# Kernel tuning notes

Hardware: AMD Instinct MI355X
Metric: run time of the kernel (lower is better)

The kernel has to match this reference:

```python
import jax, jax.numpy as jnp
import numpy as np

N = 50000
H = 8          # heads
C = 10         # out channels per head
F_IN = 128
NEG_SLOPE = 0.2


def _glorot(key, shape, fan_in):
    return jax.random.normal(key, shape, dtype=jnp.float32) / np.sqrt(fan_in)


def setup_inputs() -> dict:
    key = jax.random.key(0)
    ks = jax.random.split(key, 16)
    x = jax.random.normal(ks[0], (N, F_IN), dtype=jnp.float32)
    edge_index = jax.random.randint(ks[1], (2, 1600000), 0, N, dtype=jnp.int64)
    inp = {"x": x, "edge_index": edge_index}
    dims = [F_IN, H * C, H * C]  # input dim of each of the 3 layers
    k = 2
    for i, din in enumerate(dims):
        inp[f"Wl{i}"] = _glorot(ks[k + 0], (din, H * C), din)
        inp[f"Wr{i}"] = _glorot(ks[k + 1], (din, H * C), din)
        inp[f"att{i}"] = _glorot(ks[k + 2], (H, C), C)
        inp[f"b{i}"] = jnp.zeros((H * C,), dtype=jnp.float32)
        k += 3
    return inp


def gatv2_layer(x, Wl, Wr, att, b, src, dst):
    # GATv2Conv (PyG defaults): separate lin_l/lin_r, e = att . leaky_relu(xl_j + xr_i),
    # segment softmax over incoming edges, scatter-add of alpha * xl_j, concat heads + bias.
    n = x.shape[0]
    xl = (x @ Wl).reshape(n, H, C)
    xr = (x @ Wr).reshape(n, H, C)
    e = jax.nn.leaky_relu(xl[src] + xr[dst], NEG_SLOPE)      # [E, H, C]
    score = jnp.einsum('ehc,hc->eh', e, att)                 # [E, H]
    smax = jax.ops.segment_max(score, dst, num_segments=n)   # [N, H]
    ex = jnp.exp(score - smax[dst])
    denom = jax.ops.segment_sum(ex, dst, num_segments=n)
    alpha = ex / (denom[dst] + 1e-16)                        # [E, H]
    out = jax.ops.segment_sum(alpha[:, :, None] * xl[src], dst, num_segments=n)
    return out.reshape(n, H * C) + b


def reference(x, edge_index, Wl0, Wr0, att0, b0, Wl1, Wr1, att1, b1, Wl2, Wr2, att2, b2):
    n = x.shape[0]
    # add_self_loops=True (PyG default)
    loop = jnp.arange(n, dtype=edge_index.dtype)
    src = jnp.concatenate([edge_index[0], loop])
    dst = jnp.concatenate([edge_index[1], loop])
    params = [(Wl0, Wr0, att0, b0), (Wl1, Wr1, att1, b1), (Wl2, Wr2, att2, b2)]
    for Wl, Wr, att, b in params:
        x = jax.nn.elu(gatv2_layer(x, Wl, Wr, att, b, src, dst))
    return x
```

## Files before the change

kernel.cpp:

```cpp
#include <hip/hip_runtime.h>
#include <hip/hip_bf16.h>
#include <hip/hip_fp16.h>

#define N_NODES 50000
#define HEADS 8
#define CHANS 10
#define HC 80
#define PADH 12
#define PHL 96
#define F_IN 128
#define E_EDGES 1600000
#define E_TOT (E_EDGES + N_NODES)
#define NEG_SLOPE 0.2f
#define NBUCK 3125
#define NAGG 6250
#define NCHUNK 128
#define CHUNK ((E_TOT + NCHUNK - 1) / NCHUNK)
#define XS_STRIDE 40
#define WS_STRIDE 40

typedef _Float16 f16x8 __attribute__((ext_vector_type(8)));
typedef float f32x4 __attribute__((ext_vector_type(4)));

#if __has_builtin(__builtin_amdgcn_fdot2) && __has_builtin(__builtin_elementwise_max)
#define USE_PK_SCORE 1
typedef _Float16 h2 __attribute__((ext_vector_type(2)));
#else
#define USE_PK_SCORE 0
#endif

__device__ inline void load_edge(const void* ei, int is64, int e, int& src, int& dst) {
    if (e < E_EDGES) {
        if (is64) {
            src = ((const int*)ei)[2 * e];
            dst = ((const int*)ei)[2 * (E_EDGES + e)];
        } else {
            src = ((const int*)ei)[e];
            dst = ((const int*)ei)[E_EDGES + e];
        }
    } else {
        src = dst = e - E_EDGES;
    }
}

__device__ inline int load_dst(const void* ei, int is64, int e) {
    if (e < E_EDGES) {
        if (is64) return ((const int*)ei)[2 * (E_EDGES + e)];
        return ((const int*)ei)[E_EDGES + e];
    }
    return e - E_EDGES;
}

__device__ inline int detect_is64(const void* ei, int tid, int* s_flag) {
    if (tid < 64) {
        const int* p = (const int*)ei;
        bool ok = (p[2 * tid + 1] == 0) && (p[2 * (tid + 64) + 1] == 0);
        unsigned long long m = __ballot(ok);
        if (tid == 0) *s_flag = (m == ~0ull) ? 1 : 0;
    }
    return 0;
}

__global__ __launch_bounds__(256) void hist_kernel(
        const void* ei, int* __restrict__ hist, int* __restrict__ bcount) {
    __shared__ int h[NBUCK];
    __shared__ int s_is64;
    int tid = threadIdx.x;
    for (int i = tid; i < NBUCK; i += 256) h[i] = 0;
    detect_is64(ei, tid, &s_is64);
    __syncthreads();
    int is64 = s_is64;
    int blk = blockIdx.x;
    int e0 = blk * CHUNK, e1 = min(e0 + CHUNK, E_TOT);
    for (int e = e0 + tid; e < e1; e += 4 * 256) {
        int d[4]; int cnt = 0;
        #pragma unroll
        for (int u = 0; u < 4; u++) {
            int ee = e + u * 256;
            if (ee < e1) { d[u] = load_dst(ei, is64, ee); cnt = u + 1; }
        }
        #pragma unroll
        for (int u = 0; u < 4; u++)
            if (u < cnt) atomicAdd(&h[d[u] >> 4], 1);
    }
    __syncthreads();
    for (int i = tid; i < NBUCK; i += 256) {
        int v = h[i];
        int old = v ? atomicAdd(&bcount[i], v) : 0;
        hist[blk * NBUCK + i] = old;
    }
}

__global__ void scan_total_kernel(const int* __restrict__ total, int* __restrict__ bbase) {
    __shared__ int wsum[16];
    __shared__ int wpre[16];
    __shared__ int carry;
    int tid = threadIdx.x;
    int lane = tid & 63, w = tid >> 6;
    if (tid == 0) carry = 0;
    __syncthreads();
    for (int base = 0; base < NBUCK; base += 1024) {
        int idx = base + tid;
        int v = (idx < NBUCK) ? total[idx] : 0;
        int sv = v;
        #pragma unroll
        for (int off = 1; off < 64; off <<= 1) {
            int t = __shfl_up(sv, off, 64);
            if (lane >= off) sv += t;
        }
        if (lane == 63) wsum[w] = sv;
        __syncthreads();
        if (w == 0) {
            int s = (lane < 16) ? wsum[lane] : 0;
            #pragma unroll
            for (int off = 1; off < 16; off <<= 1) {
                int t = __shfl_up(s, off, 64);
                if (lane >= off) s += t;
            }
            if (lane < 16) wpre[lane] = s;
        }
        __syncthreads();
        int pre = carry + ((w > 0) ? wpre[w - 1] : 0);
        if (idx < NBUCK) bbase[idx] = pre + sv - v;
        __syncthreads();
        if (tid == 0) carry += wpre[15];
        __syncthreads();
    }
}

__global__ __launch_bounds__(256) void scatter_sort_kernel(
        const void* ei, const int* __restrict__ hist, const int* __restrict__ bbase,
        int* __restrict__ tmp) {
    __shared__ int cur[NBUCK];
    __shared__ int s_is64;
    int tid = threadIdx.x;
    int blk = blockIdx.x;
    for (int i = tid; i < NBUCK; i += 256)
        cur[i] = bbase[i] + hist[blk * NBUCK + i];
    detect_is64(ei, tid, &s_is64);
    __syncthreads();
    int is64 = s_is64;
    int e0 = blk * CHUNK, e1 = min(e0 + CHUNK, E_TOT);
    for (int e = e0 + tid; e < e1; e += 4 * 256) {
        int s[4], d[4]; int cnt = 0;
        #pragma unroll
        for (int u = 0; u < 4; u++) {
            int ee = e + u * 256;
            if (ee < e1) { load_edge(ei, is64, ee, s[u], d[u]); cnt = u + 1; }
        }
        #pragma unroll
        for (int u = 0; u < 4; u++) {
            if (u < cnt) {
                int pos = atomicAdd(&cur[d[u] >> 4], 1);
                tmp[pos] = (s[u] << 4) | (d[u] & 15);
            }
        }
    }
}

__global__ __launch_bounds__(256) void node_sort_kernel(
        const int* __restrict__ tmp, const int* __restrict__ bbase,
        const int* __restrict__ total,
        int* __restrict__ adj, int* __restrict__ nstart, int* __restrict__ deg) {
    __shared__ int h16[16];
    __shared__ int st16[16];
    __shared__ int cur16[16];
    int tid = threadIdx.x;
    int b = blockIdx.x;
    int base = bbase[b];
    int n = total[b];
    if (tid < 16) h16[tid] = 0;
    __syncthreads();
    for (int k = tid; k < n; k += 256)
        atomicAdd(&h16[tmp[base + k] & 15], 1);
    __syncthreads();
    if (tid == 0) {
        int run = 0;
        #pragma unroll
        for (int c = 0; c < 16; c++) { st16[c] = run; cur16[c] = run; run += h16[c]; }
    }
    __syncthreads();
    for (int k = tid; k < n; k += 256) {
        int p = tmp[base + k];
        int pos = atomicAdd(&cur16[p & 15], 1);
        adj[base + pos] = p >> 4;
    }
    if (tid < 16) {
        nstart[b * 16 + tid] = base + st16[tid];
        deg[b * 16 + tid] = h16[tid];
    }
}

__global__ __launch_bounds__(256) void deghist_kernel(
        const int* __restrict__ deg, int* __restrict__ dh) {
    __shared__ int h[256];
    h[threadIdx.x] = 0;
    __syncthreads();
    int i = blockIdx.x * 256 + threadIdx.x;
    if (i < N_NODES) atomicAdd(&h[min(deg[i], 255)], 1);
    __syncthreads();
    if (h[threadIdx.x]) atomicAdd(&dh[threadIdx.x], h[threadIdx.x]);
}

__global__ void degscan_kernel(const int* __restrict__ dh, int* __restrict__ dcur) {
    __shared__ int s[256];
    int tid = threadIdx.x;
    int idx = 255 - tid;
    int own = dh[idx];
    s[tid] = own;
    __syncthreads();
    for (int off = 1; off < 256; off <<= 1) {
        int t = (tid >= off) ? s[tid - off] : 0;
        __syncthreads();
        s[tid] += t;
        __syncthreads();
    }
    dcur[idx] = s[tid] - own;
}

__global__ __launch_bounds__(256) void degscatter_kernel(
        const int* __restrict__ deg, int* __restrict__ dcur, int* __restrict__ perm) {
    __shared__ int h[256];
    __shared__ int res[256];
    __shared__ int lc[256];
    int tid = threadIdx.x;
    h[tid] = 0; lc[tid] = 0;
    __syncthreads();
    int i = blockIdx.x * 256 + tid;
    int d = (i < N_NODES) ? min(deg[i], 255) : -1;
    if (d >= 0) atomicAdd(&h[d], 1);
    __syncthreads();
    res[tid] = h[tid] ? atomicAdd(&dcur[tid], h[tid]) : 0;
    __syncthreads();
    if (d >= 0) {
        int off = atomicAdd(&lc[d], 1);
        perm[res[d] + off] = i;
    }
}

__global__ void wconv_kernel(const float* __restrict__ Wl0, const float* __restrict__ Wr0,
                             const float* __restrict__ Wl1, const float* __restrict__ Wr1,
                             const float* __restrict__ Wl2, const float* __restrict__ Wr2,
                             __half* __restrict__ wt) {
    int g = blockIdx.x;
    int layer = g / 160, c = g - layer * 160;
    int kp = threadIdx.x;
    const float* Wl = (layer == 0) ? Wl0 : (layer == 1) ? Wl1 : Wl2;
    const float* Wr = (layer == 0) ? Wr0 : (layer == 1) ? Wr1 : Wr2;
    const float* W = (c < 80) ? Wl : Wr;
    int cc = (c < 80) ? c : c - 80;
    float v = 0.f;
    if (layer == 0) {
        if (kp < F_IN) v = W[kp * 80 + cc];
    } else {
        int hh = kp / PADH, c2 = kp - hh * PADH;
        if (kp < PHL && c2 < CHANS)
            v = W[(hh * CHANS + c2) * 80 + cc];
    }
    wt[(size_t)g * 128 + kp] = __float2half_rn(v);
}

__global__ __launch_bounds__(256) void gemm_mfma_kernel(
        const void* __restrict__ xin, int in_fp16, int nkt,
        const __half* __restrict__ wt,
        __half* __restrict__ xlh, float* __restrict__ xr) {
    __shared__ __half xs[128 * XS_STRIDE];
    __shared__ __half ws[160 * WS_STRIDE];
    int tid = threadIdx.x;
    int n0 = blockIdx.x * 128;
    int w = tid >> 6, lane = tid & 63;
    int quad = lane >> 4, r = lane & 15;

    f32x4 acc[2][10];
    #pragma unroll
    for (int nt = 0; nt < 2; nt++)
        #pragma unroll
        for (int t = 0; t < 10; t++) acc[nt][t] = (f32x4){0.f, 0.f, 0.f, 0.f};

    int snode = tid >> 1;
    int sk = (tid & 1) * 16;
    int sg = n0 + snode;

    for (int kt = 0; kt < nkt; kt++) {
        f16x8 xv0 = (f16x8){0, 0, 0, 0, 0, 0, 0, 0}, xv1 = xv0;
        if (sg < N_NODES) {
            if (in_fp16) {
                const uint4* p = (const uint4*)((const __half*)xin + (size_t)sg * PHL + kt * 32 + sk);
                xv0 = __builtin_bit_cast(f16x8, p[0]);
                xv1 = __builtin_bit_cast(f16x8, p[1]);
            } else {
                const float4* p = (const float4*)((const float*)xin + (size_t)sg * F_IN + kt * 32 + sk);
                float4 f0 = p[0], f1 = p[1], f2 = p[2], f3 = p[3];
                xv0[0] = (_Float16)f0.x; xv0[1] = (_Float16)f0.y;
                xv0[2] = (_Float16)f0.z; xv0[3] = (_Float16)f0.w;
                xv0[4] = (_Float16)f1.x; xv0[5] = (_Float16)f1.y;
                xv0[6] = (_Float16)f1.z; xv0[7] = (_Float16)f1.w;
                xv1[0] = (_Float16)f2.x; xv1[1] = (_Float16)f2.y;
                xv1[2] = (_Float16)f2.z; xv1[3] = (_Float16)f2.w;
                xv1[4] = (_Float16)f3.x; xv1[5] = (_Float16)f3.y;
                xv1[6] = (_Float16)f3.z; xv1[7] = (_Float16)f3.w;
            }
        }
        __syncthreads();
        *(uint4*)(&xs[snode * XS_STRIDE + sk]) = __builtin_bit_cast(uint4, xv0);
        *(uint4*)(&xs[snode * XS_STRIDE + sk + 8]) = __builtin_bit_cast(uint4, xv1);
        for (int u = tid; u < 640; u += 256) {
            int c = u >> 2, k8 = (u & 3) * 8;
            uint4 wv = *(const uint4*)(wt + c * 128 + kt * 32 + k8);
            *(uint4*)(&ws[c * WS_STRIDE + k8]) = wv;
        }
        __syncthreads();
        #pragma unroll
        for (int nt = 0; nt < 2; nt++) {
            f16x8 a = __builtin_bit_cast(f16x8,
                         *(const uint4*)(&xs[(w * 32 + nt * 16 + r) * XS_STRIDE + quad * 8]));
            #pragma unroll
            for (int ct = 0; ct < 10; ct++) {
                f16x8 bf = __builtin_bit_cast(f16x8,
                              *(const uint4*)(&ws[(ct * 16 + r) * WS_STRIDE + quad * 8]));
                acc[nt][ct] = __builtin_amdgcn_mfma_f32_16x16x32_f16(a, bf, acc[nt][ct], 0, 0, 0);
            }
        }
    }
    #pragma unroll
    for (int nt = 0; nt < 2; nt++) {
        #pragma unroll
        for (int ct = 0; ct < 10; ct++) {
            int col = ct * 16 + r;
            #pragma unroll
            for (int reg = 0; reg < 4; reg++) {
                int node = n0 + w * 32 + nt * 16 + quad * 4 + reg;
                if (node < N_NODES) {
                    float v = acc[nt][ct][reg];
                    if (col < 80) {
                        int hh = col / 10, cc = col - hh * 10;
                        xlh[(size_t)node * PHL + hh * PADH + cc] = __float2half_rn(v);
                    } else {
                        xr[(size_t)node * HC + (col - 80)] = v;
                    }
                }
            }
        }
    }
}

__device__ inline void cvt10(uint2 a, uint2 b, uint2 c, float* v) {
    __half2 h;
    h = *(__half2*)&a.x; v[0] = __low2float(h); v[1] = __high2float(h);
    h = *(__half2*)&a.y; v[2] = __low2float(h); v[3] = __high2float(h);
    h = *(__half2*)&b.x; v[4] = __low2float(h); v[5] = __high2float(h);
    h = *(__half2*)&b.y; v[6] = __low2float(h); v[7] = __high2float(h);
    h = *(__half2*)&c.x; v[8] = __low2float(h); v[9] = __high2float(h);
}

__global__ __launch_bounds__(256, 4) void agg_kernel(
        const __half* __restrict__ xlh, const float* __restrict__ xr,
        const float* __restrict__ att, const float* __restrict__ bias,
        const int* __restrict__ nstart, const int* __restrict__ deg,
        const int* __restrict__ adj, const int* __restrict__ perm,
        __half* __restrict__ ybuf, float* __restrict__ yout) {
    int tid = threadIdx.x;
    int b = blockIdx.x;
    int h = tid & 7;
    int split = (tid >> 3) & 3;
    int i_local = tid >> 5;
    int node = perm[b * 8 + i_local];

    int s0 = nstart[node];
    int dg = deg[node];
    int base = dg >> 2, rem = dg & 3;
    int cnt = base + (split < rem ? 1 : 0);
    int k0 = s0 + split * base + min(split, rem);

#if USE_PK_SCORE
    h2 xrh[5], atth[5];
    #pragma unroll
    for (int p = 0; p < 5; p++) {
        xrh[p] = (h2){(_Float16)xr[(size_t)node * HC + h * CHANS + 2 * p],
                      (_Float16)xr[(size_t)node * HC + h * CHANS + 2 * p + 1]};
        atth[p] = (h2){(_Float16)att[h * CHANS + 2 * p],
                       (_Float16)att[h * CHANS + 2 * p + 1]};
    }
    const h2 k02 = {(_Float16)NEG_SLOPE, (_Float16)NEG_SLOPE};
    auto score_pk = [&](uint2 a, uint2 bq, uint2 cq) {
        unsigned int wv[5] = {a.x, a.y, bq.x, bq.y, cq.x};
        float s = 0.f;
        #pragma unroll
        for (int p = 0; p < 5; p++) {
            h2 v = __builtin_bit_cast(h2, wv[p]);
            h2 t = v + xrh[p];
            h2 tl = __builtin_elementwise_max(t, t * k02);
            s = __builtin_amdgcn_fdot2(tl, atth[p], s, false);
        }
        return s;
    };
#else
    float xr_c[CHANS], att_c[CHANS];
    #pragma unroll
    for (int c = 0; c < CHANS; c++) {
        xr_c[c]  = xr[(size_t)node * HC + h * CHANS + c];
        att_c[c] = att[h * CHANS + c];
    }
    auto score_pk = [&](uint2 a, uint2 bq, uint2 cq) {
        float v[CHANS];
        cvt10(a, bq, cq, v);
        float s = 0.f;
        #pragma unroll
        for (int c = 0; c < CHANS; c++) {
            float t = v[c] + xr_c[c];
            t = (t > 0.f) ? t : NEG_SLOPE * t;
            s += att_c[c] * t;
        }
        return s;
    };
#endif

    float m = -1e30f, l = 0.f;
    float acc[CHANS];
    #pragma unroll
    for (int c = 0; c < CHANS; c++) acc[c] = 0.f;

    int kk = 0;
    for (; kk + 8 <= cnt; kk += 8) {
        uint2 ra[8], rb[8], rc[8];
        #pragma unroll
        for (int r = 0; r < 8; r++) {
            int j = adj[k0 + kk + r];
            const uint2* p = (const uint2*)(xlh + (size_t)j * PHL + h * PADH);
            ra[r] = p[0]; rb[r] = p[1]; rc[r] = p[2];
        }
        float sc[8];
        #pragma unroll
        for (int r = 0; r < 8; r++) sc[r] = score_pk(ra[r], rb[r], rc[r]);
        float mb = m;
        #pragma unroll
        for (int r = 0; r < 8; r++) mb = fmaxf(mb, sc[r]);
        float scale = __expf(m - mb);
        float ps = 0.f;
        #pragma unroll
        for (int r = 0; r < 8; r++) { sc[r] = __expf(sc[r] - mb); ps += sc[r]; }
        l = l * scale + ps;
        #pragma unroll
        for (int c = 0; c < CHANS; c++) acc[c] *= scale;
        #pragma unroll
        for (int r = 0; r < 8; r++) {
            float v[CHANS];
            cvt10(ra[r], rb[r], rc[r], v);
            #pragma unroll
            for (int c = 0; c < CHANS; c++) acc[c] += sc[r] * v[c];
        }
        m = mb;
    }
    for (; kk < cnt; kk++) {
        int j = adj[k0 + kk];
        const uint2* p = (const uint2*)(xlh + (size_t)j * PHL + h * PADH);
        uint2 a = p[0], bq = p[1], cq = p[2];
        float s = score_pk(a, bq, cq);
        float v[CHANS];
        cvt10(a, bq, cq, v);
        float mn = fmaxf(m, s);
        float scale = __expf(m - mn);
        float pp = __expf(s - mn);
        l = l * scale + pp;
        #pragma unroll
        for (int c = 0; c < CHANS; c++) acc[c] = acc[c] * scale + pp * v[c];
        m = mn;
    }

    #pragma unroll
    for (int stride = 8; stride <= 16; stride <<= 1) {
        float m2 = __shfl_xor(m, stride, 64);
        float l2 = __shfl_xor(l, stride, 64);
        float mn = fmaxf(m, m2);
        float sc1 = __expf(m - mn), sc2 = __expf(m2 - mn);
        l = l * sc1 + l2 * sc2;
        #pragma unroll
        for (int c = 0; c < CHANS; c++) {
            float a2 = __shfl_xor(acc[c], stride, 64);
            acc[c] = acc[c] * sc1 + a2 * sc2;
        }
        m = mn;
    }
    if (split == 0) {
        float inv = 1.f / (l + 1e-16f);
        float z[CHANS];
        #pragma unroll
        for (int c = 0; c < CHANS; c++) {
            float t = acc[c] * inv + bias[h * CHANS + c];
            z[c] = (t > 0.f) ? t : (__expf(t) - 1.f);
        }
        if (yout) {
            #pragma unroll
            for (int c = 0; c < CHANS; c++)
                yout[(size_t)node * HC + h * CHANS + c] = z[c];
        } else {
            __half2 h0 = __halves2half2(__float2half_rn(z[0]), __float2half_rn(z[1]));
            __half2 h1 = __halves2half2(__float2half_rn(z[2]), __float2half_rn(z[3]));
            __half2 h2v = __halves2half2(__float2half_rn(z[4]), __float2half_rn(z[5]));
            __half2 h3 = __halves2half2(__float2half_rn(z[6]), __float2half_rn(z[7]));
            __half2 h4 = __halves2half2(__float2half_rn(z[8]), __float2half_rn(z[9]));
            __half2 h5 = __halves2half2(__half(0.f), __half(0.f));
            uint2* dst = (uint2*)(ybuf + (size_t)node * PHL + h * PADH);
            dst[0] = make_uint2(*(unsigned*)&h0, *(unsigned*)&h1);
            dst[1] = make_uint2(*(unsigned*)&h2v, *(unsigned*)&h3);
            dst[2] = make_uint2(*(unsigned*)&h4, *(unsigned*)&h5);
        }
    }
}

extern "C" void kernel_launch(void* const* d_in, const int* in_sizes, int n_in,
                              void* d_out, int out_size, void* d_ws, size_t ws_size,
                              hipStream_t stream) {
    const float* x_in = (const float*)d_in[0];
    const void*  ei   = d_in[1];
    const float* Wl[3] = {(const float*)d_in[2], (const float*)d_in[6],  (const float*)d_in[10]};
    const float* Wr[3] = {(const float*)d_in[3], (const float*)d_in[7],  (const float*)d_in[11]};
    const float* At[3] = {(const float*)d_in[4], (const float*)d_in[8],  (const float*)d_in[12]};
    const float* Bi[3] = {(const float*)d_in[5], (const float*)d_in[9],  (const float*)d_in[13]};
    float* out = (float*)d_out;

    char* ws = (char*)d_ws;
    size_t off = 0;
    auto alloc = [&](size_t bytes) {
        void* p = ws + off;
        off += (bytes + 255) & ~(size_t)255;
        return p;
    };
    __half* xlh   = (__half*)alloc((size_t)N_NODES * PHL * sizeof(__half));
    float*  xr    = (float*)alloc((size_t)N_NODES * HC * sizeof(float));
    __half* buf16 = (__half*)alloc((size_t)N_NODES * PHL * sizeof(__half));
    __half* wt    = (__half*)alloc((size_t)3 * 160 * 128 * sizeof(__half));
    int*   tmp    = (int*)alloc((size_t)E_TOT * sizeof(int));
    int*   adj    = (int*)alloc((size_t)E_TOT * sizeof(int));
    int*   hist   = (int*)alloc((size_t)NCHUNK * NBUCK * sizeof(int));
    int*   bcount = (int*)alloc((size_t)NBUCK * sizeof(int));
    int*   dh     = (int*)alloc(256 * sizeof(int));
    int*   bbase  = (int*)alloc((size_t)NBUCK * sizeof(int));
    int*   nstart = (int*)alloc((size_t)N_NODES * sizeof(int));
    int*   deg    = (int*)alloc((size_t)N_NODES * sizeof(int));
    int*   perm   = (int*)alloc((size_t)N_NODES * sizeof(int));
    int*   dcur   = (int*)alloc(256 * sizeof(int));

    hipMemsetAsync(bcount, 0, (size_t)((char*)dh - (char*)bcount) + 1024, stream);
    wconv_kernel<<<480, 128, 0, stream>>>(Wl[0], Wr[0], Wl[1], Wr[1], Wl[2], Wr[2], wt);
    hist_kernel<<<NCHUNK, 256, 0, stream>>>(ei, hist, bcount);
    scan_total_kernel<<<1, 1024, 0, stream>>>(bcount, bbase);
    scatter_sort_kernel<<<NCHUNK, 256, 0, stream>>>(ei, hist, bbase, tmp);
    node_sort_kernel<<<NBUCK, 256, 0, stream>>>(tmp, bbase, bcount, adj, nstart, deg);
    int nblocks = (N_NODES + 255) / 256;
    deghist_kernel<<<nblocks, 256, 0, stream>>>(deg, dh);
    degscan_kernel<<<1, 256, 0, stream>>>(dh, dcur);
    degscatter_kernel<<<nblocks, 256, 0, stream>>>(deg, dcur, perm);

    int gemm_blocks = (N_NODES + 127) / 128;
    const void* cur = (const void*)x_in;
    int in_fp16 = 0;
    for (int layer = 0; layer < 3; layer++) {
        int nkt = (layer == 0) ? 4 : 3;
        gemm_mfma_kernel<<<gemm_blocks, 256, 0, stream>>>(
            cur, in_fp16, nkt, wt + (size_t)layer * 160 * 128, xlh, xr);
        __half* ybuf = (layer == 2) ? nullptr : buf16;
        float*  yout = (layer == 2) ? out : nullptr;
        agg_kernel<<<NAGG, 256, 0, stream>>>(xlh, xr, At[layer], Bi[layer],
                                             nstart, deg, adj, perm, ybuf, yout);
        cur = (const void*)buf16;
        in_fp16 = 1;
    }
}
```

Baseline: 371.1 us.

## Halve edge splits per node in aggregation and fuse preprocessing kernels

The aggregation kernel now handles 16 nodes per block with 2 edge splits per (node, head) instead of 8 nodes with 4 splits. It adds a 4-wide unrolled tail loop and needs only one cross-lane shuffle-merge step. Separately, the weight conversion is folded into the histogram kernel as extra blocks, and the degree histogram is computed inside node_sort, which removes two kernel launches. The trade-off is longer serial edge loops per thread, which could hurt latency hiding on high-degree nodes, in exchange for less reduction overhead and better utilisation of threads on low-degree nodes.

New measurement: 448.1 us. 1.21x slower.

```diff
diff --git a/kernel.cpp b/kernel.cpp
--- a/kernel.cpp
+++ b/kernel.cpp
@@ -13,7 +13,6 @@
 #define E_TOT (E_EDGES + N_NODES)
 #define NEG_SLOPE 0.2f
 #define NBUCK 3125
-#define NAGG 6250
 #define NCHUNK 128
 #define CHUNK ((E_TOT + NCHUNK - 1) / NCHUNK)
 #define XS_STRIDE 40
@@ -61,16 +60,41 @@
     return 0;
 }
 
-__global__ __launch_bounds__(256) void hist_kernel(
-        const void* ei, int* __restrict__ hist, int* __restrict__ bcount) {
+__global__ __launch_bounds__(256) void hist_wconv_kernel(
+        const void* ei, int* __restrict__ hist, int* __restrict__ bcount,
+        const float* __restrict__ Wl0, const float* __restrict__ Wr0,
+        const float* __restrict__ Wl1, const float* __restrict__ Wr1,
+        const float* __restrict__ Wl2, const float* __restrict__ Wr2,
+        __half* __restrict__ wt) {
+    int blk = blockIdx.x;
+    int tid = threadIdx.x;
+    if (blk >= NCHUNK) {
+        if (tid < 128) {
+            int g = blk - NCHUNK;
+            int layer = g / 160, c = g - layer * 160;
+            int kp = tid;
+            const float* Wl = (layer == 0) ? Wl0 : (layer == 1) ? Wl1 : Wl2;
+            const float* Wr = (layer == 0) ? Wr0 : (layer == 1) ? Wr1 : Wr2;
+            const float* W = (c < 80) ? Wl : Wr;
+            int cc = (c < 80) ? c : c - 80;
+            float v = 0.f;
+            if (layer == 0) {
+                if (kp < F_IN) v = W[kp * 80 + cc];
+            } else {
+                int hh = kp / PADH, c2 = kp - hh * PADH;
+                if (kp < PHL && c2 < CHANS)
+                    v = W[(hh * CHANS + c2) * 80 + cc];
+            }
+            wt[(size_t)g * 128 + kp] = __float2half_rn(v);
+        }
+        return;
+    }
     __shared__ int h[NBUCK];
     __shared__ int s_is64;
-    int tid = threadIdx.x;
     for (int i = tid; i < NBUCK; i += 256) h[i] = 0;
     detect_is64(ei, tid, &s_is64);
     __syncthreads();
     int is64 = s_is64;
-    int blk = blockIdx.x;
     int e0 = blk * CHUNK, e1 = min(e0 + CHUNK, E_TOT);
     for (int e = e0 + tid; e < e1; e += 4 * 256) {
         int d[4]; int cnt = 0;
@@ -161,7 +185,8 @@
 __global__ __launch_bounds__(256) void node_sort_kernel(
         const int* __restrict__ tmp, const int* __restrict__ bbase,
         const int* __restrict__ total,
-        int* __restrict__ adj, int* __restrict__ nstart, int* __restrict__ deg) {
+        int* __restrict__ adj, int* __restrict__ nstart, int* __restrict__ deg,
+        int* __restrict__ dh) {
     __shared__ int h16[16];
     __shared__ int st16[16];
     __shared__ int cur16[16];
@@ -188,18 +213,8 @@
     if (tid < 16) {
         nstart[b * 16 + tid] = base + st16[tid];
         deg[b * 16 + tid] = h16[tid];
-    }
-}
-
-__global__ __launch_bounds__(256) void deghist_kernel(
-        const int* __restrict__ deg, int* __restrict__ dh) {
-    __shared__ int h[256];
-    h[threadIdx.x] = 0;
-    __syncthreads();
-    int i = blockIdx.x * 256 + threadIdx.x;
-    if (i < N_NODES) atomicAdd(&h[min(deg[i], 255)], 1);
-    __syncthreads();
-    if (h[threadIdx.x]) atomicAdd(&dh[threadIdx.x], h[threadIdx.x]);
+        atomicAdd(&dh[min(h16[tid], 255)], 1);
+    }
 }
 
 __global__ void degscan_kernel(const int* __restrict__ dh, int* __restrict__ dcur) {
@@ -236,28 +251,6 @@
         int off = atomicAdd(&lc[d], 1);
         perm[res[d] + off] = i;
     }
-}
-
-__global__ void wconv_kernel(const float* __restrict__ Wl0, const float* __restrict__ Wr0,
-                             const float* __restrict__ Wl1, const float* __restrict__ Wr1,
-                             const float* __restrict__ Wl2, const float* __restrict__ Wr2,
-                             __half* __restrict__ wt) {
-    int g = blockIdx.x;
-    int layer = g / 160, c = g - layer * 160;
-    int kp = threadIdx.x;
-    const float* Wl = (layer == 0) ? Wl0 : (layer == 1) ? Wl1 : Wl2;
-    const float* Wr = (layer == 0) ? Wr0 : (layer == 1) ? Wr1 : Wr2;
-    const float* W = (c < 80) ? Wl : Wr;
-    int cc = (c < 80) ? c : c - 80;
-    float v = 0.f;
-    if (layer == 0) {
-        if (kp < F_IN) v = W[kp * 80 + cc];
-    } else {
-        int hh = kp / PADH, c2 = kp - hh * PADH;
-        if (kp < PHL && c2 < CHANS)
-            v = W[(hh * CHANS + c2) * 80 + cc];
-    }
-    wt[(size_t)g * 128 + kp] = __float2half_rn(v);
 }
 
 __global__ __launch_bounds__(256) void gemm_mfma_kernel(
@@ -362,15 +355,15 @@
     int tid = threadIdx.x;
     int b = blockIdx.x;
     int h = tid & 7;
-    int split = (tid >> 3) & 3;
-    int i_local = tid >> 5;
-    int node = perm[b * 8 + i_local];
+    int split = (tid >> 3) & 1;
+    int i_local = tid >> 4;
+    int node = perm[b * 16 + i_local];
 
     int s0 = nstart[node];
     int dg = deg[node];
-    int base = dg >> 2, rem = dg & 3;
-    int cnt = base + (split < rem ? 1 : 0);
-    int k0 = s0 + split * base + min(split, rem);
+    int cnt0 = (dg + 1) >> 1;
+    int cnt = split ? (dg - cnt0) : cnt0;
+    int k0 = s0 + split * cnt0;
 
 #if USE_PK_SCORE
     h2 xrh[5], atth[5];
@@ -444,6 +437,36 @@
         for (int c = 0; c < CHANS; c++) acc[c] *= scale;
         #pragma unroll
         for (int r = 0; r < 8; r++) {
+            float v[CHANS];
+            cvt10(ra[r], rb[r], rc[r], v);
+            #pragma unroll
+            for (int c = 0; c < CHANS; c++) acc[c] += sc[r] * v[c];
+        }
+        m = mb;
+    }
+    for (; kk + 4 <= cnt; kk += 4) {
+        uint2 ra[4], rb[4], rc[4];
+        #pragma unroll
+        for (int r = 0; r < 4; r++) {
+            int j = adj[k0 + kk + r];
+            const uint2* p = (const uint2*)(xlh + (size_t)j * PHL + h * PADH);
+            ra[r] = p[0]; rb[r] = p[1]; rc[r] = p[2];
+        }
+        float sc[4];
+        #pragma unroll
+        for (int r = 0; r < 4; r++) sc[r] = score_pk(ra[r], rb[r], rc[r]);
+        float mb = m;
+        #pragma unroll
+        for (int r = 0; r < 4; r++) mb = fmaxf(mb, sc[r]);
+        float scale = __expf(m - mb);
+        float ps = 0.f;
+        #pragma unroll
+        for (int r = 0; r < 4; r++) { sc[r] = __expf(sc[r] - mb); ps += sc[r]; }
+        l = l * scale + ps;
+        #pragma unroll
+        for (int c = 0; c < CHANS; c++) acc[c] *= scale;
+        #pragma unroll
+        for (int r = 0; r < 4; r++) {
             float v[CHANS];
             cvt10(ra[r], rb[r], rc[r], v);
             #pragma unroll
@@ -467,16 +490,15 @@
         m = mn;
     }
 
-    #pragma unroll
-    for (int stride = 8; stride <= 16; stride <<= 1) {
-        float m2 = __shfl_xor(m, stride, 64);
-        float l2 = __shfl_xor(l, stride, 64);
+    {
+        float m2 = __shfl_xor(m, 8, 64);
+        float l2 = __shfl_xor(l, 8, 64);
         float mn = fmaxf(m, m2);
         float sc1 = __expf(m - mn), sc2 = __expf(m2 - mn);
         l = l * sc1 + l2 * sc2;
         #pragma unroll
         for (int c = 0; c < CHANS; c++) {
-            float a2 = __shfl_xor(acc[c], stride, 64);
+            float a2 = __shfl_xor(acc[c], 8, 64);
             acc[c] = acc[c] * sc1 + a2 * sc2;
         }
         m = mn;
@@ -542,14 +564,13 @@
     int*   dcur   = (int*)alloc(256 * sizeof(int));
 
     hipMemsetAsync(bcount, 0, (size_t)((char*)dh - (char*)bcount) + 1024, stream);
-    wconv_kernel<<<480, 128, 0, stream>>>(Wl[0], Wr[0], Wl[1], Wr[1], Wl[2], Wr[2], wt);
-    hist_kernel<<<NCHUNK, 256, 0, stream>>>(ei, hist, bcount);
+    hist_wconv_kernel<<<NCHUNK + 480, 256, 0, stream>>>(
+        ei, hist, bcount, Wl[0], Wr[0], Wl[1], Wr[1], Wl[2], Wr[2], wt);
     scan_total_kernel<<<1, 1024, 0, stream>>>(bcount, bbase);
     scatter_sort_kernel<<<NCHUNK, 256, 0, stream>>>(ei, hist, bbase, tmp);
-    node_sort_kernel<<<NBUCK, 256, 0, stream>>>(tmp, bbase, bcount, adj, nstart, deg);
+    node_sort_kernel<<<NBUCK, 256, 0, stream>>>(tmp, bbase, bcount, adj, nstart, deg, dh);
+    degscan_kernel<<<1, 256, 0, stream>>>(dh, dcur);
     int nblocks = (N_NODES + 255) / 256;
-    deghist_kernel<<<nblocks, 256, 0, stream>>>(deg, dh);
-    degscan_kernel<<<1, 256, 0, stream>>>(dh, dcur);
     degscatter_kernel<<<nblocks, 256, 0, stream>>>(deg, dcur, perm);
 
     int gemm_blocks = (N_NODES + 127) / 128;
@@ -561,8 +582,8 @@
             cur, in_fp16, nkt, wt + (size_t)layer * 160 * 128, xlh, xr);
         __half* ybuf = (layer == 2) ? nullptr : buf16;
         float*  yout = (layer == 2) ? out : nullptr;
-        agg_kernel<<<NAGG, 256, 0, stream>>>(xlh, xr, At[layer], Bi[layer],
-                                             nstart, deg, adj, perm, ybuf, yout);
+        agg_kernel<<<NBUCK, 256, 0, stream>>>(xlh, xr, At[layer], Bi[layer],
+                                              nstart, deg, adj, perm, ybuf, yout);
         cur = (const void*)buf16;
         in_fp16 = 1;
     }
```
